# Kernel tuning notes

Hardware: AMD Instinct MI355X
Metric: run time of the kernel (lower is better)

## Reference

```python
import jax, jax.numpy as jnp
import numpy as np

B, S, D_IN, D_OUT = 4, 2048, 1024, 1024


def setup_inputs() -> dict:
    key = jax.random.key(0)
    ks = jax.random.split(key, 6)
    scale = 1.0 / np.sqrt(D_IN)
    return {
        "inputs_for_keys": jax.random.normal(ks[0], (B, S, D_IN), jnp.float32),
        "inputs_for_values": jax.random.normal(ks[1], (B, S, D_IN), jnp.float32),
        "inputs_for_queries": jax.random.normal(ks[2], (B, S, D_IN), jnp.float32),
        "WK": jax.random.uniform(ks[3], (D_IN, D_OUT), jnp.float32, -scale, scale),
        "WQ": jax.random.uniform(ks[4], (D_IN, D_OUT), jnp.float32, -scale, scale),
        "WV": jax.random.uniform(ks[5], (D_IN, D_OUT), jnp.float32, -scale, scale),
    }


def reference(inputs_for_keys, inputs_for_values, inputs_for_queries, WK, WQ, WV):
    # QKV projections: [B,S,Din] @ [Din,Dout] -> [B,S,Dout]
    keys = jnp.einsum("bsd,de->bse", inputs_for_keys, WK)
    values = jnp.einsum("bsd,de->bse", inputs_for_values, WV)
    queries = jnp.einsum("bsd,de->bse", inputs_for_queries, WQ)
    d_k = keys.shape[-1]
    # scaled scores [B,S,S]
    scores = jnp.einsum("bqe,bke->bqk", queries, keys) / jnp.sqrt(jnp.float32(d_k))
    # causal mask: position k > q gets -inf (strictly upper triangular)
    q_idx = jnp.arange(S)[:, None]
    k_idx = jnp.arange(S)[None, :]
    scores = jnp.where(k_idx > q_idx, -jnp.inf, scores)
    att = jax.nn.softmax(scores, axis=-1)
    out = jnp.einsum("bqk,bke->bqe", att, values)  # [B,S,Dout]
    return out
```

## Files before the change

### kernel.cpp

```cpp
#include <hip/hip_runtime.h>
#include <stdint.h>


typedef __attribute__((ext_vector_type(8))) short short8;
typedef __attribute__((ext_vector_type(8))) unsigned short ushort8;
typedef __attribute__((ext_vector_type(4))) float f32x4;

__device__ __forceinline__ unsigned short f2bf(float f) {
  union { float f; unsigned u; } v; v.f = f;
  unsigned u = v.u + 0x7FFFu + ((v.u >> 16) & 1u);
  return (unsigned short)(u >> 16);
}
__device__ __forceinline__ float bf2f(unsigned short h) {
  union { unsigned u; float f; } v; v.u = ((unsigned)h) << 16;
  return v.f;
}

__device__ __forceinline__ void gload16(const void* g, void* l) {
  __builtin_amdgcn_global_load_lds(
      (const __attribute__((address_space(1))) unsigned int*)g,
      (__attribute__((address_space(3))) unsigned int*)l, 16, 0, 0);
}

template<int N> __device__ __forceinline__ void vmwait() {
  static_assert(N >= 0 && N <= 8, "vmcnt range");
  if constexpr (N == 0) asm volatile("s_waitcnt vmcnt(0)" ::: "memory");
  else if constexpr (N == 1) asm volatile("s_waitcnt vmcnt(1)" ::: "memory");
  else if constexpr (N == 2) asm volatile("s_waitcnt vmcnt(2)" ::: "memory");
  else if constexpr (N == 3) asm volatile("s_waitcnt vmcnt(3)" ::: "memory");
  else if constexpr (N == 4) asm volatile("s_waitcnt vmcnt(4)" ::: "memory");
  else if constexpr (N == 5) asm volatile("s_waitcnt vmcnt(5)" ::: "memory");
  else if constexpr (N == 6) asm volatile("s_waitcnt vmcnt(6)" ::: "memory");
  else if constexpr (N == 7) asm volatile("s_waitcnt vmcnt(7)" ::: "memory");
  else asm volatile("s_waitcnt vmcnt(8)" ::: "memory");
}
__device__ __forceinline__ void barrier_() { asm volatile("s_barrier" ::: "memory"); }
__device__ __forceinline__ void lgkm0() { asm volatile("s_waitcnt lgkmcnt(0)" ::: "memory"); }

__global__ __launch_bounds__(256)
void cvt3_bf16(const float* __restrict__ Xq, const float* __restrict__ Xk,
               const float* __restrict__ Xv,
               unsigned short* __restrict__ Oq, unsigned short* __restrict__ Ok,
               unsigned short* __restrict__ Ov) {
  const int bx = blockIdx.x;
  const int op = bx >> 12, r = bx & 4095;
  const float* in = op == 0 ? Xq : op == 1 ? Xk : Xv;
  unsigned short* out = op == 0 ? Oq : op == 1 ? Ok : Ov;
  const long i = ((long)r * 256 + threadIdx.x) * 8;
  float4 a = *(const float4*)(in + i);
  float4 b = *(const float4*)(in + i + 4);
  ushort8 rr;
  rr[0] = f2bf(a.x); rr[1] = f2bf(a.y); rr[2] = f2bf(a.z); rr[3] = f2bf(a.w);
  rr[4] = f2bf(b.x); rr[5] = f2bf(b.y); rr[6] = f2bf(b.z); rr[7] = f2bf(b.w);
  *(ushort8*)(out + i) = rr;
}

__global__ __launch_bounds__(256)
void wtrans3(const float* __restrict__ WQ, const float* __restrict__ WK,
             const float* __restrict__ WV,
             unsigned short* __restrict__ WQT, unsigned short* __restrict__ WKT,
             unsigned short* __restrict__ WVT) {
  const int z = blockIdx.z;
  const float* W = z == 0 ? WQ : z == 1 ? WK : WV;
  unsigned short* WT = z == 0 ? WQT : z == 1 ? WKT : WVT;
  const float scale = z == 0 ? 0.03125f : 1.0f;
  __shared__ float t[32][33];
  const int bk = blockIdx.x * 32, be = blockIdx.y * 32;
  const int tx = threadIdx.x, ty = threadIdx.y;
#pragma unroll
  for (int j = 0; j < 32; j += 8)
    t[ty + j][tx] = W[(long)(bk + ty + j) * 1024 + (be + tx)];
  __syncthreads();
#pragma unroll
  for (int j = 0; j < 32; j += 8)
    WT[(long)(be + ty + j) * 1024 + (bk + tx)] = f2bf(t[tx][ty + j] * scale);
}

template<typename CT, int MF, int NF>
__device__ __forceinline__ void gemm_body(const unsigned short* __restrict__ A,
                                          const unsigned short* __restrict__ B,
                                          CT* __restrict__ C,
                                          int bm, int bn, int kmax,
                                          int lda, int ldb, int ldc) {
  constexpr int BM = MF * 32, BN = NF * 64;
  constexpr int LA = BM / 128, LB = BN / 128;
  constexpr int V = 2 * LA + LB;
  __shared__ __align__(16) unsigned short Al[2 * 2 * BM * 32];
  __shared__ __align__(16) unsigned short Bl[2 * 2 * BN * 32];

  const int tid = threadIdx.x;
  const int lane = tid & 63, wid = tid >> 6;
  const int wr = wid >> 2, wc = wid & 3;
  const int fr = lane & 15, fq = lane >> 4;
  const int srow = tid >> 2;
  const int scol = (((tid & 3) ^ ((tid >> 3) & 3)) << 3);
  const int m0 = bm * BM, n0 = bn * BN;
  const int nt = kmax >> 6;

  f32x4 acc[MF][NF] = {};

  const unsigned short* As = A + (long)(m0 + srow) * lda + scol;
  const unsigned short* Bs = B + (long)(n0 + srow) * ldb + scol;
  char* AL = (char*)Al;
  char* BL = (char*)Bl;

  auto stageA = [&](int b, int h, int kt) {
#pragma unroll
    for (int l = 0; l < LA; ++l)
      gload16(As + (long)l * 128 * lda + kt * 64 + h * 32,
              AL + b * (BM * 128) + h * (BM * 64) + l * 8192 + tid * 16);
  };
  auto stageB = [&](int b, int h, int kt) {
#pragma unroll
    for (int l = 0; l < LB; ++l)
      gload16(Bs + (long)l * 128 * ldb + kt * 64 + h * 32,
              BL + b * (BN * 128) + h * (BN * 64) + l * 8192 + tid * 16);
  };

  const int aoff = (wr * (BM / 2) + fr) * 64 + ((fq ^ ((fr >> 1) & 3)) << 4);
  const int boff = (wc * (BN / 4) + fr) * 64 + ((fq ^ ((fr >> 1) & 3)) << 4);
  auto ardf = [&](int b, int kk, int m) -> short8 {
    return *(const short8*)(AL + b * (BM * 128) + kk * (BM * 64) + aoff + m * 1024);
  };
  auto brdf = [&](int b, int kk, int n) -> short8 {
    return *(const short8*)(BL + b * (BN * 128) + kk * (BN * 64) + boff + n * 1024);
  };

  stageA(0, 0, 0); stageB(0, 0, 0); stageA(0, 1, 0); stageB(0, 1, 0);

  for (int u = 0; u < nt; ++u) {
    const int cb = u & 1, nb = cb ^ 1;
    const bool pf = (u + 1 < nt);
    lgkm0();
    barrier_();
    if (pf) { stageA(nb, 0, u + 1); vmwait<V>(); }
    else    { vmwait<LA + LB>(); }
    barrier_();
    short8 bfr[NF], af[MF / 2];
#pragma unroll
    for (int n = 0; n < NF; ++n) bfr[n] = brdf(cb, 0, n);
#pragma unroll
    for (int m = 0; m < MF / 2; ++m) af[m] = ardf(cb, 0, m);
    if (pf) stageB(nb, 0, u + 1);
    __builtin_amdgcn_s_setprio(1);
#pragma unroll
    for (int m = 0; m < MF / 2; ++m)
#pragma unroll
      for (int n = 0; n < NF; ++n)
        acc[m][n] = __builtin_amdgcn_mfma_f32_16x16x32_bf16(af[m], bfr[n], acc[m][n], 0, 0, 0);
    __builtin_amdgcn_s_setprio(0);
#pragma unroll
    for (int m = 0; m < MF / 2; ++m) af[m] = ardf(cb, 0, MF / 2 + m);
    if (pf) stageA(nb, 1, u + 1);
    __builtin_amdgcn_s_setprio(1);
#pragma unroll
    for (int m = 0; m < MF / 2; ++m)
#pragma unroll
      for (int n = 0; n < NF; ++n)
        acc[MF / 2 + m][n] =
            __builtin_amdgcn_mfma_f32_16x16x32_bf16(af[m], bfr[n], acc[MF / 2 + m][n], 0, 0, 0);
    __builtin_amdgcn_s_setprio(0);
    if (pf) vmwait<V>(); else vmwait<0>();
    barrier_();
#pragma unroll
    for (int n = 0; n < NF; ++n) bfr[n] = brdf(cb, 1, n);
#pragma unroll
    for (int m = 0; m < MF / 2; ++m) af[m] = ardf(cb, 1, m);
    if (pf) stageB(nb, 1, u + 1);
    __builtin_amdgcn_s_setprio(1);
#pragma unroll
    for (int m = 0; m < MF / 2; ++m)
#pragma unroll
      for (int n = 0; n < NF; ++n)
        acc[m][n] = __builtin_amdgcn_mfma_f32_16x16x32_bf16(af[m], bfr[n], acc[m][n], 0, 0, 0);
    __builtin_amdgcn_s_setprio(0);
#pragma unroll
    for (int m = 0; m < MF / 2; ++m) af[m] = ardf(cb, 1, MF / 2 + m);
    __builtin_amdgcn_s_setprio(1);
#pragma unroll
    for (int m = 0; m < MF / 2; ++m)
#pragma unroll
      for (int n = 0; n < NF; ++n)
        acc[MF / 2 + m][n] =
            __builtin_amdgcn_mfma_f32_16x16x32_bf16(af[m], bfr[n], acc[MF / 2 + m][n], 0, 0, 0);
    __builtin_amdgcn_s_setprio(0);
  }

#pragma unroll
  for (int m = 0; m < MF; ++m) {
    const int row = m0 + wr * (BM / 2) + m * 16 + fq * 4;
#pragma unroll
    for (int n = 0; n < NF; ++n) {
      const int col = n0 + wc * (BN / 4) + n * 16 + fr;
#pragma unroll
      for (int r = 0; r < 4; ++r) {
        float v = acc[m][n][r];
        if constexpr (sizeof(CT) == 2)
          C[(long)(row + r) * ldc + col] = (CT)f2bf(v);
        else
          C[(long)(row + r) * ldc + col] = (CT)v;
      }
    }
  }
}

__global__ __launch_bounds__(512, 2)
void qkv_gemm(const unsigned short* __restrict__ Xq, const unsigned short* __restrict__ WQT,
              unsigned short* __restrict__ Q,
              const unsigned short* __restrict__ Xk, const unsigned short* __restrict__ WKT,
              unsigned short* __restrict__ Kk,
              const unsigned short* __restrict__ WVT, const unsigned short* __restrict__ Xv,
              unsigned short* __restrict__ VT) {
  const int id = (blockIdx.x & 7) * 48 + (blockIdx.x >> 3);
  const unsigned short *A, *B;
  unsigned short* C;
  int bm, bn, ldc = 1024;
  if (id < 128)      { A = Xq;  B = WQT; C = Q;  bm = id >> 2;        bn = id & 3; }
  else if (id < 256) { int r = id - 128; A = Xk;  B = WKT; C = Kk; bm = r >> 2;  bn = r & 3; }
  else               { int r = id - 256; A = WVT; B = Xv;  C = VT; bm = r >> 5;  bn = r & 31; ldc = 8192; }
  gemm_body<unsigned short, 8, 4>(A, B, C, bm, bn, 1024, 1024, 1024, ldc);
}

__global__ __launch_bounds__(512, 2)
void scores_gemm(const unsigned short* __restrict__ Q, const unsigned short* __restrict__ K,
                 unsigned short* __restrict__ S) {
  const int id = (blockIdx.x & 7) * 32 + (blockIdx.x >> 3);
  const int bz = id >> 6, r = id & 63, bm = r >> 3, bn = r & 7;
  if (bn > bm) return;
  gemm_body<unsigned short, 8, 4>(Q + (long)bz * 2048 * 1024, K + (long)bz * 2048 * 1024,
                                  S + (long)bz * 2048 * 2048, bm, bn, 1024, 1024, 1024, 2048);
}

__global__ __launch_bounds__(512, 4)
void pv_gemm(const unsigned short* __restrict__ P, const unsigned short* __restrict__ VT,
             float* __restrict__ O) {
  const int b = blockIdx.x;
  int bm, r;
  if (b < 256) { bm = 15 - (b >> 5); r = b & 31; }
  else         { bm = (b - 256) >> 5; r = b & 31; }
  const int bn = r & 7, bz = r >> 3;
  gemm_body<float, 4, 2>(P + (long)bz * 2048 * 2048, VT + (long)bz * 2048,
                         O + (long)bz * 2048 * 1024, bm, bn, (bm + 1) * 128,
                         2048, 8192, 1024);
}

__global__ __launch_bounds__(256)
void softmax_causal(unsigned short* __restrict__ P) {
  const int row = blockIdx.x;
  const int q = row & 2047;
  unsigned short* p = P + (long)row * 2048;
  const int nfill = ((q >> 7) + 1) << 7;
  const int tid = threadIdx.x;
  const int lane = tid & 63, wid = tid >> 6;
  const int i0 = tid * 8;
  __shared__ float red[8];

  ushort8 v8 = *(const ushort8*)(p + i0);
  float v[8];
  float lmax = -3.0e38f;
#pragma unroll
  for (int j = 0; j < 8; ++j) {
    float f = bf2f(v8[j]);
    f = (i0 + j <= q) ? f : -3.0e38f;
    v[j] = f;
    lmax = fmaxf(lmax, f);
  }
#pragma unroll
  for (int off = 1; off < 64; off <<= 1)
    lmax = fmaxf(lmax, __shfl_xor(lmax, off));
  if (lane == 0) red[wid] = lmax;
  __syncthreads();
  const float mx = fmaxf(fmaxf(red[0], red[1]), fmaxf(red[2], red[3]));

  float lsum = 0.f;
#pragma unroll
  for (int j = 0; j < 8; ++j) {
    float e = __expf(v[j] - mx);
    v[j] = e;
    lsum += e;
  }
#pragma unroll
  for (int off = 1; off < 64; off <<= 1)
    lsum += __shfl_xor(lsum, off);
  if (lane == 0) red[4 + wid] = lsum;
  __syncthreads();
  const float inv = 1.0f / (red[4] + red[5] + red[6] + red[7]);

  if (i0 < nfill) {
    ushort8 r;
#pragma unroll
    for (int j = 0; j < 8; ++j)
      r[j] = (i0 + j <= q) ? f2bf(v[j] * inv) : (unsigned short)0;
    *(ushort8*)(p + i0) = r;
  }
}

extern "C" void kernel_launch(void* const* d_in, const int* in_sizes, int n_in,
                              void* d_out, int out_size, void* d_ws, size_t ws_size,
                              hipStream_t stream) {
  const float* Xk = (const float*)d_in[0];
  const float* Xv = (const float*)d_in[1];
  const float* Xq = (const float*)d_in[2];
  const float* WK = (const float*)d_in[3];
  const float* WQ = (const float*)d_in[4];
  const float* WV = (const float*)d_in[5];
  float* out = (float*)d_out;

  unsigned short* ws = (unsigned short*)d_ws;
  const long NE = 8L * 1024 * 1024;
  unsigned short* Xqb = ws + 0 * NE;
  unsigned short* Xkb = ws + 1 * NE;
  unsigned short* Xvb = ws + 2 * NE;
  unsigned short* Qb  = ws + 3 * NE;
  unsigned short* Kb  = ws + 4 * NE;
  unsigned short* VTb = ws + 5 * NE;
  unsigned short* WQT = ws + 6 * NE;
  unsigned short* WKT = WQT + 1024 * 1024;
  unsigned short* WVT = WKT + 1024 * 1024;
  unsigned short* Sc  = ws;

  dim3 b256(256), b512(512);
  cvt3_bf16<<<12288, b256, 0, stream>>>(Xq, Xk, Xv, Xqb, Xkb, Xvb);
  wtrans3<<<dim3(32, 32, 3), dim3(32, 8), 0, stream>>>(WQ, WK, WV, WQT, WKT, WVT);
  qkv_gemm<<<384, b512, 0, stream>>>(Xqb, WQT, Qb, Xkb, WKT, Kb, WVT, Xvb, VTb);
  scores_gemm<<<256, b512, 0, stream>>>(Qb, Kb, Sc);
  softmax_causal<<<8192, b256, 0, stream>>>(Sc);
  pv_gemm<<<512, b512, 0, stream>>>(Sc, VTb, out);
}
```

Before: 177.2 us.

## Rebalance QKV projection into one wave and skip masked softmax loads

```diff
diff --git a/kernel.cpp b/kernel.cpp
--- a/kernel.cpp
+++ b/kernel.cpp
@@ -81,12 +81,11 @@
                                           const unsigned short* __restrict__ B,
                                           CT* __restrict__ C,
                                           int bm, int bn, int kmax,
-                                          int lda, int ldb, int ldc) {
+                                          int lda, int ldb, int ldc,
+                                          char* AL, char* BL) {
   constexpr int BM = MF * 32, BN = NF * 64;
   constexpr int LA = BM / 128, LB = BN / 128;
   constexpr int V = 2 * LA + LB;
-  __shared__ __align__(16) unsigned short Al[2 * 2 * BM * 32];
-  __shared__ __align__(16) unsigned short Bl[2 * 2 * BN * 32];
 
   const int tid = threadIdx.x;
   const int lane = tid & 63, wid = tid >> 6;
@@ -101,8 +100,6 @@
 
   const unsigned short* As = A + (long)(m0 + srow) * lda + scol;
   const unsigned short* Bs = B + (long)(n0 + srow) * ldb + scol;
-  char* AL = (char*)Al;
-  char* BL = (char*)Bl;
 
   auto stageA = [&](int b, int h, int kt) {
 #pragma unroll
@@ -205,35 +202,41 @@
 }
 
 __global__ __launch_bounds__(512, 2)
-void qkv_gemm(const unsigned short* __restrict__ Xq, const unsigned short* __restrict__ WQT,
-              unsigned short* __restrict__ Q,
-              const unsigned short* __restrict__ Xk, const unsigned short* __restrict__ WKT,
-              unsigned short* __restrict__ Kk,
-              const unsigned short* __restrict__ WVT, const unsigned short* __restrict__ Xv,
-              unsigned short* __restrict__ VT) {
-  const int id = (blockIdx.x & 7) * 48 + (blockIdx.x >> 3);
-  const unsigned short *A, *B;
-  unsigned short* C;
-  int bm, bn, ldc = 1024;
-  if (id < 128)      { A = Xq;  B = WQT; C = Q;  bm = id >> 2;        bn = id & 3; }
-  else if (id < 256) { int r = id - 128; A = Xk;  B = WKT; C = Kk; bm = r >> 2;  bn = r & 3; }
-  else               { int r = id - 256; A = WVT; B = Xv;  C = VT; bm = r >> 5;  bn = r & 31; ldc = 8192; }
-  gemm_body<unsigned short, 8, 4>(A, B, C, bm, bn, 1024, 1024, 1024, ldc);
+void qkvt_gemm(const unsigned short* __restrict__ Xq, const unsigned short* __restrict__ WQT,
+               unsigned short* __restrict__ Q,
+               const unsigned short* __restrict__ Xk, const unsigned short* __restrict__ WKT,
+               unsigned short* __restrict__ Kk,
+               const unsigned short* __restrict__ WVT, const unsigned short* __restrict__ Xv,
+               unsigned short* __restrict__ VT) {
+  __shared__ __align__(16) char pool[131072];
+  const int id = (blockIdx.x & 7) * 32 + (blockIdx.x >> 3);
+  if (id < 128)
+    gemm_body<unsigned short, 8, 4>(Xq, WQT, Q, id >> 2, id & 3, 1024,
+                                    1024, 1024, 1024, pool, pool + 65536);
+  else
+    gemm_body<unsigned short, 8, 4>(Xk, WKT, Kk, (id - 128) >> 2, id & 3, 1024,
+                                    1024, 1024, 1024, pool, pool + 65536);
+  __syncthreads();
+  gemm_body<unsigned short, 4, 4>(WVT, Xv, VT, id >> 5, id & 31, 1024,
+                                  1024, 1024, 8192, pool, pool + 32768);
 }
 
 __global__ __launch_bounds__(512, 2)
 void scores_gemm(const unsigned short* __restrict__ Q, const unsigned short* __restrict__ K,
                  unsigned short* __restrict__ S) {
+  __shared__ __align__(16) char pool[131072];
   const int id = (blockIdx.x & 7) * 32 + (blockIdx.x >> 3);
   const int bz = id >> 6, r = id & 63, bm = r >> 3, bn = r & 7;
   if (bn > bm) return;
   gemm_body<unsigned short, 8, 4>(Q + (long)bz * 2048 * 1024, K + (long)bz * 2048 * 1024,
-                                  S + (long)bz * 2048 * 2048, bm, bn, 1024, 1024, 1024, 2048);
+                                  S + (long)bz * 2048 * 2048, bm, bn, 1024,
+                                  1024, 1024, 2048, pool, pool + 65536);
 }
 
 __global__ __launch_bounds__(512, 4)
 void pv_gemm(const unsigned short* __restrict__ P, const unsigned short* __restrict__ VT,
              float* __restrict__ O) {
+  __shared__ __align__(16) char pool[65536];
   const int b = blockIdx.x;
   int bm, r;
   if (b < 256) { bm = 15 - (b >> 5); r = b & 31; }
@@ -241,7 +244,7 @@
   const int bn = r & 7, bz = r >> 3;
   gemm_body<float, 4, 2>(P + (long)bz * 2048 * 2048, VT + (long)bz * 2048,
                          O + (long)bz * 2048 * 1024, bm, bn, (bm + 1) * 128,
-                         2048, 8192, 1024);
+                         2048, 8192, 1024, pool, pool + 32768);
 }
 
 __global__ __launch_bounds__(256)
@@ -255,15 +258,20 @@
   const int i0 = tid * 8;
   __shared__ float red[8];
 
-  ushort8 v8 = *(const ushort8*)(p + i0);
   float v[8];
   float lmax = -3.0e38f;
-#pragma unroll
-  for (int j = 0; j < 8; ++j) {
-    float f = bf2f(v8[j]);
-    f = (i0 + j <= q) ? f : -3.0e38f;
-    v[j] = f;
-    lmax = fmaxf(lmax, f);
+  if (i0 <= q) {
+    ushort8 v8 = *(const ushort8*)(p + i0);
+#pragma unroll
+    for (int j = 0; j < 8; ++j) {
+      float f = bf2f(v8[j]);
+      f = (i0 + j <= q) ? f : -3.0e38f;
+      v[j] = f;
+      lmax = fmaxf(lmax, f);
+    }
+  } else {
+#pragma unroll
+    for (int j = 0; j < 8; ++j) v[j] = -3.0e38f;
   }
 #pragma unroll
   for (int off = 1; off < 64; off <<= 1)
@@ -322,7 +330,7 @@
   dim3 b256(256), b512(512);
   cvt3_bf16<<<12288, b256, 0, stream>>>(Xq, Xk, Xv, Xqb, Xkb, Xvb);
   wtrans3<<<dim3(32, 32, 3), dim3(32, 8), 0, stream>>>(WQ, WK, WV, WQT, WKT, WVT);
-  qkv_gemm<<<384, b512, 0, stream>>>(Xqb, WQT, Qb, Xkb, WKT, Kb, WVT, Xvb, VTb);
+  qkvt_gemm<<<256, b512, 0, stream>>>(Xqb, WQT, Qb, Xkb, WKT, Kb, WVT, Xvb, VTb);
   scores_gemm<<<256, b512, 0, stream>>>(Qb, Kb, Sc);
   softmax_causal<<<8192, b256, 0, stream>>>(Sc);
   pv_gemm<<<512, b512, 0, stream>>>(Sc, VTb, out);
```

Result: faster. 157.2 us (-11.3%).
